# Optimization experiments

Hardware: AMD Instinct MI355X
Metric: run time of the kernel (lower is better)

## Reference

```python
import jax, jax.numpy as jnp
import numpy as np

N = 100000
E = 600000
IN_DIM = 128
OUT_DIM = 256
BN_EPS = 1e-5


def setup_inputs() -> dict:
    key = jax.random.key(0)
    ks = jax.random.split(key, 12)
    x = jax.random.normal(ks[0], (N, IN_DIM), dtype=jnp.float32)
    edge_index = jax.random.randint(ks[1], (2, E), 0, N, dtype=jnp.int64)
    s1 = 1.0 / np.sqrt(IN_DIM)
    s2 = 1.0 / np.sqrt(OUT_DIM)
    return {
        "x": x,
        "edge_index": edge_index,
        "eps": jnp.zeros((), dtype=jnp.float32),  # GINConv eps init = 0
        "W1": jax.random.uniform(ks[2], (IN_DIM, OUT_DIM), jnp.float32, -s1, s1),
        "b1": jnp.zeros((OUT_DIM,), jnp.float32),
        "W2": jax.random.uniform(ks[3], (OUT_DIM, OUT_DIM), jnp.float32, -s2, s2),
        "b2": jnp.zeros((OUT_DIM,), jnp.float32),
        "gamma": jnp.ones((OUT_DIM,), jnp.float32),
        "beta": jnp.zeros((OUT_DIM,), jnp.float32),
        "run_mean": jnp.zeros((OUT_DIM,), jnp.float32),
        "run_var": jnp.ones((OUT_DIM,), jnp.float32),
        "Wp": jax.random.uniform(ks[4], (IN_DIM, OUT_DIM), jnp.float32, -s1, s1),
        "bp": jnp.zeros((OUT_DIM,), jnp.float32),
    }


def reference(x, edge_index, eps, W1, b1, W2, b2, gamma, beta, run_mean, run_var, Wp, bp):
    src, dst = edge_index[0], edge_index[1]
    # GIN aggregation: sum_{j in N(i)} x_j  (scatter-add of source features to dst)
    agg = jax.ops.segment_sum(x[src], dst, num_segments=N)
    h = (1.0 + eps) * x + agg            # [N, in_dim]
    # 2-layer MLP (nn1)
    h = jax.nn.relu(h @ W1 + b1) @ W2 + b2   # [N, out_dim]
    # BatchNorm1d (eval mode: running stats); dropout = identity (eval)
    h = (h - run_mean) * jax.lax.rsqrt(run_var + BN_EPS) * gamma + beta
    # residual with projection (in_dim != out_dim)
    return h + x @ Wp + bp
```

## Files before the change

kernel.cpp:

```cpp
#include <hip/hip_runtime.h>

#define N_ 100000
#define E_ 600000
#define IND_ 128
#define OUTD_ 256
#define NT_ (N_/16)
#define NB_ 98
#define CASTN_ (N_*IND_/2)
#define CAST4_ (CASTN_/2)

typedef __attribute__((ext_vector_type(8))) short bf16x8;
typedef __attribute__((ext_vector_type(4))) float f32x4;
typedef __attribute__((ext_vector_type(2))) unsigned int u32x2;

static __device__ __forceinline__ unsigned f2bf_u(float f){
  union { float f; unsigned u; } v; v.f = f;
  return (v.u + 0x7fffu + ((v.u >> 16) & 1u)) >> 16;
}
static __device__ __forceinline__ unsigned pack2(float a, float b){
  return f2bf_u(a) | (f2bf_u(b) << 16);
}
static __device__ __forceinline__ float blo(unsigned u){
  union { unsigned u; float f; } v; v.u = u << 16; return v.f;
}
static __device__ __forceinline__ float bhi(unsigned u){
  union { unsigned u; float f; } v; v.u = u & 0xffff0000u; return v.f;
}
static __device__ __forceinline__ void gload_lds16(const bf16x8* g, bf16x8* l){
  __builtin_amdgcn_global_load_lds((const __attribute__((address_space(1))) void*)g,
                                   (__attribute__((address_space(3))) void*)l, 16, 0, 0);
}

__global__ void k_prep(const float* __restrict__ x,
                       const float* __restrict__ W1, const float* __restrict__ W2,
                       const float* __restrict__ Wp, const float* __restrict__ b2,
                       const float* __restrict__ gamma, const float* __restrict__ beta,
                       const float* __restrict__ mean, const float* __restrict__ var,
                       const float* __restrict__ bp,
                       const int* __restrict__ dst, int* __restrict__ deg,
                       unsigned short* __restrict__ W1s, unsigned short* __restrict__ W2s,
                       unsigned short* __restrict__ Wps,
                       float* __restrict__ scale, float* __restrict__ shift,
                       unsigned* __restrict__ xbw)
{
  int gid = blockIdx.x*256 + threadIdx.x;
  if (gid < 16384) {
    const float* W; unsigned short* Ws; int u;
    if (gid < 4096)       { W = W1; Ws = W1s; u = gid; }
    else if (gid < 12288) { W = W2; Ws = W2s; u = gid - 4096; }
    else                  { W = Wp; Ws = Wps; u = gid - 12288; }
    int l  = u & 63;
    int km = (u >> 6) & 1;
    int t  = (u >> 7) & 15;
    int q  = u >> 11;
    int kk = 2*q + km;
    int kb = kk*32 + (l >> 4)*8;
    int c  = 16*t + (l & 15);
    #pragma unroll
    for (int j = 0; j < 8; j++)
      Ws[u*8 + j] = (unsigned short)f2bf_u(W[(size_t)(kb + j)*OUTD_ + c]);
  } else if (gid < 16640) {
    int c = gid - 16384;
    float s = gamma[c] * rsqrtf(var[c] + 1e-5f);
    scale[c] = s;
    shift[c] = (b2[c] - mean[c]) * s + beta[c] + bp[c];
  } else if (gid < 16640 + CAST4_) {
    int ci = gid - 16640;
    float4 v = ((const float4*)x)[ci];
    u32x2 o; o.x = pack2(v.x, v.y); o.y = pack2(v.z, v.w);
    ((u32x2*)xbw)[ci] = o;
  } else if (gid < 16640 + CAST4_ + E_) {
    int e = gid - 16640 - CAST4_;
    atomicAdd(&deg[dst[e]], 1);
  }
}

__global__ __launch_bounds__(1024) void k_scan1(const int* __restrict__ deg,
                                                int* __restrict__ bsum, int* __restrict__ offs){
  __shared__ int red[16];
  int tid = threadIdx.x;
  int i = blockIdx.x*1024 + tid;
  int v = (i < N_) ? deg[i] : 0;
  #pragma unroll
  for (int d = 32; d; d >>= 1) v += __shfl_down(v, d);
  if ((tid & 63) == 0) red[tid >> 6] = v;
  __syncthreads();
  if (tid < 16) {
    int s = red[tid];
    #pragma unroll
    for (int d = 8; d; d >>= 1) s += __shfl_down(s, d, 16);
    if (tid == 0) bsum[blockIdx.x] = s;
  }
  if (blockIdx.x == 0 && tid == 0) offs[N_] = E_;
}

__global__ __launch_bounds__(1024) void k_scan2(const int* __restrict__ deg,
                                                const int* __restrict__ bsum, int* __restrict__ offs){
  __shared__ int bs[128];
  __shared__ int d1[1024];
  int tid = threadIdx.x;
  if (tid < 128) bs[tid] = (tid < NB_) ? bsum[tid] : 0;
  __syncthreads();
  #pragma unroll
  for (int d = 1; d < 128; d <<= 1){
    int v = (tid < 128 && tid >= d) ? bs[tid - d] : 0;
    __syncthreads();
    if (tid < 128) bs[tid] += v;
    __syncthreads();
  }
  int bprefix = (blockIdx.x > 0) ? bs[blockIdx.x - 1] : 0;
  int i = blockIdx.x*1024 + tid;
  int v = (i < N_) ? deg[i] : 0;
  d1[tid] = v;
  __syncthreads();
  #pragma unroll
  for (int d = 1; d < 1024; d <<= 1){
    int t = (tid >= d) ? d1[tid - d] : 0;
    __syncthreads();
    d1[tid] += t;
    __syncthreads();
  }
  if (i < N_) offs[i] = bprefix + d1[tid] - v;
}

__global__ void k_fill(const int* __restrict__ src, const int* __restrict__ dst,
                       const int* __restrict__ offs, int* __restrict__ cur, int* __restrict__ adj){
  int e = blockIdx.x*256 + threadIdx.x;
  if (e < E_) {
    int d = dst[e];
    int p = atomicAdd(&cur[d], 1);
    adj[offs[d] + p] = src[e];
  }
}

__global__ void k_agg(const unsigned* __restrict__ xb32, const int* __restrict__ offs,
                      const int* __restrict__ adj, const float* __restrict__ epsp,
                      unsigned* __restrict__ h0)
{
  int pair = blockIdx.x*4 + (threadIdx.x >> 6);
  int lane = threadIdx.x & 63;
  int row0 = pair*2;
  if (row0 >= N_) return;
  int b0 = offs[row0], e0 = offs[row0+1], e1 = offs[row0+2];
  int d0 = e0 - b0;
  int total = e1 - b0;
  float a0x0=0,a0y0=0,a0x1=0,a0y1=0,a0x2=0,a0y2=0,a0x3=0,a0y3=0;
  float a1x0=0,a1y0=0,a1x1=0,a1y1=0,a1x2=0,a1y2=0,a1x3=0,a1y3=0;

#define ACC(P, V, S)                                                        \
  { if ((P) < d0) { a0x##S += blo(V); a0y##S += bhi(V); }                   \
    else          { a1x##S += blo(V); a1y##S += bhi(V); } }

  for (int base = 0; base < total; base += 64){
    int cnt = min(64, total - base);
    int idx = adj[b0 + base + min(lane, cnt - 1)];
    int j = 0;
    for (; j + 8 <= cnt; j += 8){
      int n0=__shfl(idx,j+0), n1=__shfl(idx,j+1), n2=__shfl(idx,j+2), n3=__shfl(idx,j+3);
      int n4=__shfl(idx,j+4), n5=__shfl(idx,j+5), n6=__shfl(idx,j+6), n7=__shfl(idx,j+7);
      unsigned v0 = xb32[(size_t)n0*64 + lane];
      unsigned v1 = xb32[(size_t)n1*64 + lane];
      unsigned v2 = xb32[(size_t)n2*64 + lane];
      unsigned v3 = xb32[(size_t)n3*64 + lane];
      unsigned v4 = xb32[(size_t)n4*64 + lane];
      unsigned v5 = xb32[(size_t)n5*64 + lane];
      unsigned v6 = xb32[(size_t)n6*64 + lane];
      unsigned v7 = xb32[(size_t)n7*64 + lane];
      ACC(base+j+0, v0, 0) ACC(base+j+1, v1, 1) ACC(base+j+2, v2, 2) ACC(base+j+3, v3, 3)
      ACC(base+j+4, v4, 0) ACC(base+j+5, v5, 1) ACC(base+j+6, v6, 2) ACC(base+j+7, v7, 3)
    }
    for (; j + 4 <= cnt; j += 4){
      int n0=__shfl(idx,j+0), n1=__shfl(idx,j+1), n2=__shfl(idx,j+2), n3=__shfl(idx,j+3);
      unsigned v0 = xb32[(size_t)n0*64 + lane];
      unsigned v1 = xb32[(size_t)n1*64 + lane];
      unsigned v2 = xb32[(size_t)n2*64 + lane];
      unsigned v3 = xb32[(size_t)n3*64 + lane];
      ACC(base+j+0, v0, 0) ACC(base+j+1, v1, 1) ACC(base+j+2, v2, 2) ACC(base+j+3, v3, 3)
    }
    if (j + 2 <= cnt){
      int n0=__shfl(idx,j+0), n1=__shfl(idx,j+1);
      unsigned v0 = xb32[(size_t)n0*64 + lane];
      unsigned v1 = xb32[(size_t)n1*64 + lane];
      ACC(base+j+0, v0, 0) ACC(base+j+1, v1, 1)
      j += 2;
    }
    if (j < cnt){
      int n = __shfl(idx, j);
      unsigned v = xb32[(size_t)n*64 + lane];
      ACC(base+j, v, 2)
    }
  }
#undef ACC

  float k1 = 1.f + epsp[0];
  unsigned xw0 = xb32[(size_t)row0*64 + lane];
  unsigned xw1 = xb32[(size_t)(row0+1)*64 + lane];
  float a0x = (a0x0 + a0x1) + (a0x2 + a0x3);
  float a0y = (a0y0 + a0y1) + (a0y2 + a0y3);
  float a1x = (a1x0 + a1x1) + (a1x2 + a1x3);
  float a1y = (a1y0 + a1y1) + (a1y2 + a1y3);
  h0[(size_t)row0*64 + lane]     = pack2(fmaf(k1, blo(xw0), a0x), fmaf(k1, bhi(xw0), a0y));
  h0[(size_t)(row0+1)*64 + lane] = pack2(fmaf(k1, blo(xw1), a1x), fmaf(k1, bhi(xw1), a1y));
}

__global__ __launch_bounds__(256, 2) void k_mlp(const unsigned short* __restrict__ h0,
        const unsigned short* __restrict__ xb16,
        const bf16x8* __restrict__ W1s, const float* __restrict__ b1,
        const bf16x8* __restrict__ W2s, const bf16x8* __restrict__ Wps,
        const float* __restrict__ scale, const float* __restrict__ shift,
        float* __restrict__ out)
{
  __shared__ bf16x8 w[3][1024];
  __shared__ __align__(16) char trans[4][1280];
  int tid = threadIdx.x;
  int wv = tid >> 6, lane = tid & 63, g = lane >> 4, r = lane & 15;
  int tA0 = blockIdx.x*8 + wv*2;
  int tB0 = tA0 + 1;
  int tA = min(tA0, NT_ - 1);
  int tB = min(tB0, NT_ - 1);

  const bf16x8* hrowA = (const bf16x8*)(h0 + ((size_t)tA*16 + r)*IND_);
  const bf16x8* hrowB = (const bf16x8*)(h0 + ((size_t)tB*16 + r)*IND_);
  bf16x8 BA[4], BB[4];
  #pragma unroll
  for (int kk = 0; kk < 4; kk++) BA[kk] = hrowA[kk*4 + g];
  #pragma unroll
  for (int kk = 0; kk < 4; kk++) BB[kk] = hrowB[kk*4 + g];

  const bf16x8* sl[16];
  #pragma unroll
  for (int i = 0; i < 4; i++)  sl[i]      = W1s + i*1024;
  #pragma unroll
  for (int i = 0; i < 8; i++)  sl[4 + i]  = W2s + i*1024;
  #pragma unroll
  for (int i = 0; i < 4; i++)  sl[12 + i] = Wps + i*1024;

  auto STAGE = [&](int buf, const bf16x8* src){
    #pragma unroll
    for (int i = 0; i < 4; i++)
      gload_lds16(&src[i*256 + wv*64 + lane], &w[buf][i*256 + wv*64]);
  };
  f32x4 accA[16], accB[16];
  auto MF16 = [&](int buf, bf16x8 f0, bf16x8 f1, int tb, f32x4 (&acc)[16]){
    #pragma unroll
    for (int tt = 0; tt < 8; tt++)
      acc[tb+tt] = __builtin_amdgcn_mfma_f32_16x16x32_bf16(w[buf][(tt*2+0)*64 + lane], f0, acc[tb+tt], 0,0,0);
    #pragma unroll
    for (int tt = 0; tt < 8; tt++)
      acc[tb+tt] = __builtin_amdgcn_mfma_f32_16x16x32_bf16(w[buf][(tt*2+1)*64 + lane], f1, acc[tb+tt], 0,0,0);
  };
  #pragma unroll
  for (int t = 0; t < 16; t++){ accA[t] = (f32x4){0.f,0.f,0.f,0.f}; accB[t] = (f32x4){0.f,0.f,0.f,0.f}; }

  const float4* b1v = (const float4*)b1;
  auto EPI = [&](f32x4 (&acc)[16], bf16x8 (&H)[8]){
    #pragma unroll
    for (int kkh = 0; kkh < 8; kkh++){
      char* tr = &trans[wv][0];
      #pragma unroll
      for (int h = 0; h < 2; h++){
        int t = 2*kkh + h;
        float4 bb = b1v[t*4 + g];
        f32x4 a = acc[t];
        float v0 = fmaxf(a.x + bb.x, 0.f);
        float v1 = fmaxf(a.y + bb.y, 0.f);
        float v2 = fmaxf(a.z + bb.z, 0.f);
        float v3 = fmaxf(a.w + bb.w, 0.f);
        u32x2 dd; dd.x = pack2(v0, v1); dd.y = pack2(v2, v3);
        *(u32x2*)(tr + r*80 + h*32 + g*8) = dd;
      }
      H[kkh] = *(const bf16x8*)(tr + r*80 + g*16);
    }
    #pragma unroll
    for (int t = 0; t < 16; t++) acc[t] = (f32x4){0.f,0.f,0.f,0.f};
  };

#define PHASE(P, VM, FA0, FA1, FB0, FB1, TB)                       \
  { asm volatile("s_waitcnt vmcnt(" VM ")" ::: "memory");          \
    __builtin_amdgcn_s_barrier();                                  \
    if ((P) + 2 < 16) STAGE(((P)+2)%3, sl[(P)+2]);                 \
    MF16((P)%3, FA0, FA1, TB, accA);                               \
    MF16((P)%3, FB0, FB1, TB, accB); }

  STAGE(0, sl[0]);
  STAGE(1, sl[1]);

  PHASE(0,  "4", BA[0], BA[1], BB[0], BB[1], 0)
  PHASE(1,  "4", BA[0], BA[1], BB[0], BB[1], 8)
  PHASE(2,  "4", BA[2], BA[3], BB[2], BB[3], 0)
  PHASE(3,  "4", BA[2], BA[3], BB[2], BB[3], 8)

  bf16x8 HA[8], HB[8];
  EPI(accA, HA);
  EPI(accB, HB);

  PHASE(4,  "4", HA[0], HA[1], HB[0], HB[1], 0)
  PHASE(5,  "4", HA[0], HA[1], HB[0], HB[1], 8)
  PHASE(6,  "4", HA[2], HA[3], HB[2], HB[3], 0)
  PHASE(7,  "4", HA[2], HA[3], HB[2], HB[3], 8)
  PHASE(8,  "4", HA[4], HA[5], HB[4], HB[5], 0)
  PHASE(9,  "4", HA[4], HA[5], HB[4], HB[5], 8)

  const bf16x8* xrowA = (const bf16x8*)(xb16 + ((size_t)tA*16 + r)*IND_);
  const bf16x8* xrowB = (const bf16x8*)(xb16 + ((size_t)tB*16 + r)*IND_);
  bf16x8 XA[4], XB[4];
  #pragma unroll
  for (int kk = 0; kk < 4; kk++) XA[kk] = xrowA[kk*4 + g];
  #pragma unroll
  for (int kk = 0; kk < 4; kk++) XB[kk] = xrowB[kk*4 + g];

  PHASE(10, "4", HA[6], HA[7], HB[6], HB[7], 0)
  PHASE(11, "4", HA[6], HA[7], HB[6], HB[7], 8)
  PHASE(12, "4", XA[0], XA[1], XB[0], XB[1], 0)
  PHASE(13, "4", XA[0], XA[1], XB[0], XB[1], 8)
  PHASE(14, "4", XA[2], XA[3], XB[2], XB[3], 0)
  PHASE(15, "0", XA[2], XA[3], XB[2], XB[3], 8)
#undef PHASE

  const float4* sc = (const float4*)scale;
  const float4* sh = (const float4*)shift;
  if (tA0 < NT_){
    #pragma unroll
    for (int t = 0; t < 16; t++){
      float4 s = sc[t*4 + g], b = sh[t*4 + g];
      f32x4 a = accA[t];
      float4 o;
      o.x = fmaf(a.x, s.x, b.x);
      o.y = fmaf(a.y, s.y, b.y);
      o.z = fmaf(a.z, s.z, b.z);
      o.w = fmaf(a.w, s.w, b.w);
      *(float4*)(out + ((size_t)tA*16 + r)*OUTD_ + t*16 + g*4) = o;
    }
  }
  if (tB0 < NT_){
    #pragma unroll
    for (int t = 0; t < 16; t++){
      float4 s = sc[t*4 + g], b = sh[t*4 + g];
      f32x4 a = accB[t];
      float4 o;
      o.x = fmaf(a.x, s.x, b.x);
      o.y = fmaf(a.y, s.y, b.y);
      o.z = fmaf(a.z, s.z, b.z);
      o.w = fmaf(a.w, s.w, b.w);
      *(float4*)(out + ((size_t)tB*16 + r)*OUTD_ + t*16 + g*4) = o;
    }
  }
}

extern "C" void kernel_launch(void* const* d_in, const int* in_sizes, int n_in,
                              void* d_out, int out_size, void* d_ws, size_t ws_size,
                              hipStream_t stream)
{
  const float* x     = (const float*)d_in[0];
  const int*   ei    = (const int*)d_in[1];
  const float* eps   = (const float*)d_in[2];
  const float* W1    = (const float*)d_in[3];
  const float* b1    = (const float*)d_in[4];
  const float* W2    = (const float*)d_in[5];
  const float* b2    = (const float*)d_in[6];
  const float* gamma = (const float*)d_in[7];
  const float* beta  = (const float*)d_in[8];
  const float* rmean = (const float*)d_in[9];
  const float* rvar  = (const float*)d_in[10];
  const float* Wp    = (const float*)d_in[11];
  const float* bp    = (const float*)d_in[12];
  float* out = (float*)d_out;

  char* ws = (char*)d_ws; size_t off = 0;
  auto carve = [&](size_t b)->char* { char* p = ws + off; off = (off + b + 255) & ~(size_t)255; return p; };
  unsigned*       xbuf  = (unsigned*)carve((size_t)CASTN_*4);
  unsigned*       h0    = (unsigned*)carve((size_t)N_*64*4);
  unsigned short* W1s   = (unsigned short*)carve(4096*16);
  unsigned short* W2s   = (unsigned short*)carve(8192*16);
  unsigned short* Wps   = (unsigned short*)carve(4096*16);
  float*          scale = (float*)carve(256*4);
  float*          shift = (float*)carve(256*4);
  int*            deg   = (int*)carve((size_t)N_*4);
  int*            cur   = (int*)carve((size_t)N_*4);
  int*            offs  = (int*)carve((size_t)(N_+1)*4);
  int*            adj   = (int*)carve((size_t)E_*4);
  int*            bsum  = (int*)carve((size_t)NB_*4);

  size_t degpad = (((size_t)N_*4 + 255) & ~(size_t)255);
  hipMemsetAsync(deg, 0, degpad + (size_t)N_*4, stream);

  k_prep <<<(16640 + CAST4_ + E_ + 255)/256, 256, 0, stream>>>(x, W1, W2, Wp, b2, gamma, beta,
                                  rmean, rvar, bp, ei + E_, deg,
                                  W1s, W2s, Wps, scale, shift, xbuf);
  k_scan1<<<NB_, 1024, 0, stream>>>(deg, bsum, offs);
  k_scan2<<<NB_, 1024, 0, stream>>>(deg, bsum, offs);
  k_fill <<<(E_+255)/256, 256, 0, stream>>>(ei, ei + E_, offs, cur, adj);
  k_agg  <<<(N_/2+3)/4, 256, 0, stream>>>(xbuf, offs, adj, eps, h0);
  k_mlp  <<<(NT_+7)/8, 256, 0, stream>>>((const unsigned short*)h0, (const unsigned short*)xbuf,
                                         (const bf16x8*)W1s, b1, (const bf16x8*)W2s,
                                         (const bf16x8*)Wps, scale, shift, out);
}
```

Baseline: 173.4 us.

## Make MLP kernel persistent with LDS-resident weights split by output quarter

Replaces the per-block triple-buffered weight streaming with a persistent kernel where each 512-thread block loads W1 and one quarter of W2/Wp into LDS once, then loops over tiles. Each block computes only a quarter of the output columns, removing barriers and repeated weight staging per tile. In exchange the first layer (h0·W1 + ReLU) is recomputed by all four column-quarter blocks, and the h0 and x rows are reloaded four times, increasing MFMA work and memory reads.

Measured after the change: 691.2 us. +298.6%, slower.

```diff
diff --git a/kernel.cpp b/kernel.cpp
--- a/kernel.cpp
+++ b/kernel.cpp
@@ -203,57 +203,65 @@
   h0[(size_t)(row0+1)*64 + lane] = pack2(fmaf(k1, blo(xw1), a1x), fmaf(k1, bhi(xw1), a1y));
 }
 
-__global__ __launch_bounds__(256, 2) void k_mlp(const unsigned short* __restrict__ h0,
+__global__ __launch_bounds__(512) void k_mlp(const unsigned short* __restrict__ h0,
         const unsigned short* __restrict__ xb16,
         const bf16x8* __restrict__ W1s, const float* __restrict__ b1,
         const bf16x8* __restrict__ W2s, const bf16x8* __restrict__ Wps,
         const float* __restrict__ scale, const float* __restrict__ shift,
         float* __restrict__ out)
 {
-  __shared__ bf16x8 w[3][1024];
-  __shared__ __align__(16) char trans[4][1280];
+  __shared__ bf16x8 w1[4096];
+  __shared__ bf16x8 w2q[2048];
+  __shared__ bf16x8 wpq[1024];
+  __shared__ __align__(16) char trans[8][1280];
   int tid = threadIdx.x;
   int wv = tid >> 6, lane = tid & 63, g = lane >> 4, r = lane & 15;
-  int tA0 = blockIdx.x*8 + wv*2;
-  int tB0 = tA0 + 1;
-  int tA = min(tA0, NT_ - 1);
-  int tB = min(tB0, NT_ - 1);
-
-  const bf16x8* hrowA = (const bf16x8*)(h0 + ((size_t)tA*16 + r)*IND_);
-  const bf16x8* hrowB = (const bf16x8*)(h0 + ((size_t)tB*16 + r)*IND_);
-  bf16x8 BA[4], BB[4];
-  #pragma unroll
-  for (int kk = 0; kk < 4; kk++) BA[kk] = hrowA[kk*4 + g];
-  #pragma unroll
-  for (int kk = 0; kk < 4; kk++) BB[kk] = hrowB[kk*4 + g];
-
-  const bf16x8* sl[16];
-  #pragma unroll
-  for (int i = 0; i < 4; i++)  sl[i]      = W1s + i*1024;
-  #pragma unroll
-  for (int i = 0; i < 8; i++)  sl[4 + i]  = W2s + i*1024;
-  #pragma unroll
-  for (int i = 0; i < 4; i++)  sl[12 + i] = Wps + i*1024;
-
-  auto STAGE = [&](int buf, const bf16x8* src){
-    #pragma unroll
-    for (int i = 0; i < 4; i++)
-      gload_lds16(&src[i*256 + wv*64 + lane], &w[buf][i*256 + wv*64]);
-  };
-  f32x4 accA[16], accB[16];
-  auto MF16 = [&](int buf, bf16x8 f0, bf16x8 f1, int tb, f32x4 (&acc)[16]){
-    #pragma unroll
-    for (int tt = 0; tt < 8; tt++)
-      acc[tb+tt] = __builtin_amdgcn_mfma_f32_16x16x32_bf16(w[buf][(tt*2+0)*64 + lane], f0, acc[tb+tt], 0,0,0);
-    #pragma unroll
-    for (int tt = 0; tt < 8; tt++)
-      acc[tb+tt] = __builtin_amdgcn_mfma_f32_16x16x32_bf16(w[buf][(tt*2+1)*64 + lane], f1, acc[tb+tt], 0,0,0);
-  };
-  #pragma unroll
-  for (int t = 0; t < 16; t++){ accA[t] = (f32x4){0.f,0.f,0.f,0.f}; accB[t] = (f32x4){0.f,0.f,0.f,0.f}; }
+  int Q  = blockIdx.x & 3;
+  int gw = (blockIdx.x >> 2)*8 + wv;
+
+  #pragma unroll
+  for (int i = 0; i < 8; i++)
+    gload_lds16(&W1s[i*512 + wv*64 + lane], &w1[i*512 + wv*64]);
+  #pragma unroll
+  for (int rr_i = 0; rr_i < 2; rr_i++){
+    int rr = wv + rr_i*8;
+    int qp = rr >> 2, tl = rr & 3;
+    const bf16x8* src = W2s + qp*2048 + (4*Q + tl)*128;
+    gload_lds16(&src[lane],      &w2q[rr*128]);
+    gload_lds16(&src[64 + lane], &w2q[rr*128 + 64]);
+  }
+  {
+    int qp = wv >> 2, tl = wv & 3;
+    const bf16x8* src = Wps + qp*2048 + (4*Q + tl)*128;
+    gload_lds16(&src[lane],      &wpq[wv*128]);
+    gload_lds16(&src[64 + lane], &wpq[wv*128 + 64]);
+  }
+  __syncthreads();
 
   const float4* b1v = (const float4*)b1;
-  auto EPI = [&](f32x4 (&acc)[16], bf16x8 (&H)[8]){
+  const float4* sc  = (const float4*)scale;
+  const float4* sh  = (const float4*)shift;
+
+  for (int tile = gw; tile < NT_; tile += 512){
+    const bf16x8* hrow = (const bf16x8*)(h0 + ((size_t)tile*16 + r)*IND_);
+    bf16x8 B[4];
+    #pragma unroll
+    for (int kk = 0; kk < 4; kk++) B[kk] = hrow[kk*4 + g];
+
+    f32x4 acc[16];
+    #pragma unroll
+    for (int t = 0; t < 16; t++) acc[t] = (f32x4){0.f,0.f,0.f,0.f};
+    #pragma unroll
+    for (int q = 0; q < 2; q++)
+      #pragma unroll
+      for (int km = 0; km < 2; km++){
+        bf16x8 Bf = B[2*q + km];
+        #pragma unroll
+        for (int t = 0; t < 16; t++)
+          acc[t] = __builtin_amdgcn_mfma_f32_16x16x32_bf16(w1[q*2048 + (t*2+km)*64 + lane], Bf, acc[t], 0,0,0);
+      }
+
+    bf16x8 H[8];
     #pragma unroll
     for (int kkh = 0; kkh < 8; kkh++){
       char* tr = &trans[wv][0];
@@ -271,78 +279,45 @@
       }
       H[kkh] = *(const bf16x8*)(tr + r*80 + g*16);
     }
-    #pragma unroll
-    for (int t = 0; t < 16; t++) acc[t] = (f32x4){0.f,0.f,0.f,0.f};
-  };
-
-#define PHASE(P, VM, FA0, FA1, FB0, FB1, TB)                       \
-  { asm volatile("s_waitcnt vmcnt(" VM ")" ::: "memory");          \
-    __builtin_amdgcn_s_barrier();                                  \
-    if ((P) + 2 < 16) STAGE(((P)+2)%3, sl[(P)+2]);                 \
-    MF16((P)%3, FA0, FA1, TB, accA);                               \
-    MF16((P)%3, FB0, FB1, TB, accB); }
-
-  STAGE(0, sl[0]);
-  STAGE(1, sl[1]);
-
-  PHASE(0,  "4", BA[0], BA[1], BB[0], BB[1], 0)
-  PHASE(1,  "4", BA[0], BA[1], BB[0], BB[1], 8)
-  PHASE(2,  "4", BA[2], BA[3], BB[2], BB[3], 0)
-  PHASE(3,  "4", BA[2], BA[3], BB[2], BB[3], 8)
-
-  bf16x8 HA[8], HB[8];
-  EPI(accA, HA);
-  EPI(accB, HB);
-
-  PHASE(4,  "4", HA[0], HA[1], HB[0], HB[1], 0)
-  PHASE(5,  "4", HA[0], HA[1], HB[0], HB[1], 8)
-  PHASE(6,  "4", HA[2], HA[3], HB[2], HB[3], 0)
-  PHASE(7,  "4", HA[2], HA[3], HB[2], HB[3], 8)
-  PHASE(8,  "4", HA[4], HA[5], HB[4], HB[5], 0)
-  PHASE(9,  "4", HA[4], HA[5], HB[4], HB[5], 8)
-
-  const bf16x8* xrowA = (const bf16x8*)(xb16 + ((size_t)tA*16 + r)*IND_);
-  const bf16x8* xrowB = (const bf16x8*)(xb16 + ((size_t)tB*16 + r)*IND_);
-  bf16x8 XA[4], XB[4];
-  #pragma unroll
-  for (int kk = 0; kk < 4; kk++) XA[kk] = xrowA[kk*4 + g];
-  #pragma unroll
-  for (int kk = 0; kk < 4; kk++) XB[kk] = xrowB[kk*4 + g];
-
-  PHASE(10, "4", HA[6], HA[7], HB[6], HB[7], 0)
-  PHASE(11, "4", HA[6], HA[7], HB[6], HB[7], 8)
-  PHASE(12, "4", XA[0], XA[1], XB[0], XB[1], 0)
-  PHASE(13, "4", XA[0], XA[1], XB[0], XB[1], 8)
-  PHASE(14, "4", XA[2], XA[3], XB[2], XB[3], 0)
-  PHASE(15, "0", XA[2], XA[3], XB[2], XB[3], 8)
-#undef PHASE
-
-  const float4* sc = (const float4*)scale;
-  const float4* sh = (const float4*)shift;
-  if (tA0 < NT_){
-    #pragma unroll
-    for (int t = 0; t < 16; t++){
-      float4 s = sc[t*4 + g], b = sh[t*4 + g];
-      f32x4 a = accA[t];
+
+    const bf16x8* xrow = (const bf16x8*)(xb16 + ((size_t)tile*16 + r)*IND_);
+    bf16x8 XV[4];
+    #pragma unroll
+    for (int kk = 0; kk < 4; kk++) XV[kk] = xrow[kk*4 + g];
+
+    f32x4 aq[4];
+    #pragma unroll
+    for (int tl = 0; tl < 4; tl++) aq[tl] = (f32x4){0.f,0.f,0.f,0.f};
+    #pragma unroll
+    for (int qp = 0; qp < 4; qp++)
+      #pragma unroll
+      for (int km = 0; km < 2; km++){
+        bf16x8 Bf = H[2*qp + km];
+        #pragma unroll
+        for (int tl = 0; tl < 4; tl++)
+          aq[tl] = __builtin_amdgcn_mfma_f32_16x16x32_bf16(w2q[(qp*4+tl)*128 + km*64 + lane], Bf, aq[tl], 0,0,0);
+      }
+    #pragma unroll
+    for (int qp = 0; qp < 2; qp++)
+      #pragma unroll
+      for (int km = 0; km < 2; km++){
+        bf16x8 Bf = XV[2*qp + km];
+        #pragma unroll
+        for (int tl = 0; tl < 4; tl++)
+          aq[tl] = __builtin_amdgcn_mfma_f32_16x16x32_bf16(wpq[(qp*4+tl)*128 + km*64 + lane], Bf, aq[tl], 0,0,0);
+      }
+
+    #pragma unroll
+    for (int tl = 0; tl < 4; tl++){
+      int cb = (4*Q + tl)*4 + g;
+      float4 s = sc[cb], b = sh[cb];
+      f32x4 a = aq[tl];
       float4 o;
       o.x = fmaf(a.x, s.x, b.x);
       o.y = fmaf(a.y, s.y, b.y);
       o.z = fmaf(a.z, s.z, b.z);
       o.w = fmaf(a.w, s.w, b.w);
-      *(float4*)(out + ((size_t)tA*16 + r)*OUTD_ + t*16 + g*4) = o;
-    }
-  }
-  if (tB0 < NT_){
-    #pragma unroll
-    for (int t = 0; t < 16; t++){
-      float4 s = sc[t*4 + g], b = sh[t*4 + g];
-      f32x4 a = accB[t];
-      float4 o;
-      o.x = fmaf(a.x, s.x, b.x);
-      o.y = fmaf(a.y, s.y, b.y);
-      o.z = fmaf(a.z, s.z, b.z);
-      o.w = fmaf(a.w, s.w, b.w);
-      *(float4*)(out + ((size_t)tB*16 + r)*OUTD_ + t*16 + g*4) = o;
+      *(float4*)(out + ((size_t)tile*16 + r)*OUTD_ + (4*Q+tl)*16 + g*4) = o;
     }
   }
 }
@@ -391,7 +366,7 @@
   k_scan2<<<NB_, 1024, 0, stream>>>(deg, bsum, offs);
   k_fill <<<(E_+255)/256, 256, 0, stream>>>(ei, ei + E_, offs, cur, adj);
   k_agg  <<<(N_/2+3)/4, 256, 0, stream>>>(xbuf, offs, adj, eps, h0);
-  k_mlp  <<<(NT_+7)/8, 256, 0, stream>>>((const unsigned short*)h0, (const unsigned short*)xbuf,
-                                         (const bf16x8*)W1s, b1, (const bf16x8*)W2s,
-                                         (const bf16x8*)Wps, scale, shift, out);
-}
+  k_mlp  <<<256, 512, 0, stream>>>((const unsigned short*)h0, (const unsigned short*)xbuf,
+                                   (const bf16x8*)W1s, b1, (const bf16x8*)W2s,
+                                   (const bf16x8*)Wps, scale, shift, out);
+}
```
